# Performance work log

Hardware: AMD Instinct MI355X
Metric: run time of the kernel (lower is better)

## Reference

```python
import jax, jax.numpy as jnp
import numpy as np

B, C, H, W = 4, 64, 64, 64


def setup_inputs() -> dict:
    key = jax.random.key(0)
    k1, k2, k3, k4, k5 = jax.random.split(key, 5)
    return {
        "x": jax.random.normal(k1, (B, C, H, W), dtype=jnp.float32),
        "w_qkv": jax.random.normal(k2, (3 * C, C), dtype=jnp.float32) * (1.0 / np.sqrt(C)),
        "b_qkv": jax.random.normal(k3, (3 * C,), dtype=jnp.float32) * 0.02,
        "w_proj": jax.random.normal(k4, (C, C), dtype=jnp.float32) * (1.0 / np.sqrt(C)),
        "b_proj": jax.random.normal(k5, (C,), dtype=jnp.float32) * 0.02,
    }


def reference(x, w_qkv, b_qkv, w_proj, b_proj):
    b, c, h, w = x.shape
    xf = x.reshape(b, c, h * w)                                  # [B, C, N]
    # 1x1 Conv1d == per-position linear over channels
    qkv = jnp.einsum('oc,bcn->bon', w_qkv, xf) + b_qkv[None, :, None]  # [B, 3C, N]
    q, k, v = jnp.split(qkv, 3, axis=1)                          # each [B, C, N]
    scores = jnp.einsum('bcn,bcm->bnm', q, k) / (c ** 0.5)       # [B, N, N]
    attn = jax.nn.softmax(scores, axis=-1)
    out = jnp.einsum('bcm,bnm->bcn', v, attn)                    # [B, C, N]
    out = jnp.einsum('oc,bcn->bon', w_proj, out) + b_proj[None, :, None]
    return out.reshape(b, c, h, w) + x
```

## Files before the change

kernel.cpp:

```cpp
#include <hip/hip_runtime.h>

typedef __bf16 bf16x8 __attribute__((ext_vector_type(8)));
typedef __bf16 bf16x4 __attribute__((ext_vector_type(4)));
typedef float f32x4 __attribute__((ext_vector_type(4)));
typedef short s16x4 __attribute__((ext_vector_type(4)));

#define NB 4
#define NC 64
#define NN 4096
#define SPLIT 8

#define QSCALE (0.125f * 1.44269504088896340736f)

#if __has_builtin(__builtin_amdgcn_exp2f)
#define EXP2(x) __builtin_amdgcn_exp2f(x)
#else
#define EXP2(x) exp2f(x)
#endif

#define GLL16(src, dst)                                                  \
  __builtin_amdgcn_global_load_lds(                                      \
      (const __attribute__((address_space(1))) void*)(src),              \
      (__attribute__((address_space(3))) void*)(dst), 16, 0, 0)

__global__ __launch_bounds__(256) void qkv_kernel(
    const float* __restrict__ x, const float* __restrict__ wqkv,
    const float* __restrict__ bqkv,
    __bf16* __restrict__ Qg, __bf16* __restrict__ Kg, __bf16* __restrict__ Vg)
{
  const int tid = threadIdx.x;
  const int wave = tid >> 6;
  const int lane = tid & 63;
  const int quad = lane >> 4;
  const int l16 = lane & 15;
  const int b = blockIdx.y;
  const int tsel = blockIdx.z;
  const int n0 = blockIdx.x * 128 + wave * 32;
  const float wscale = (tsel == 0) ? QSCALE : 1.0f;

  bf16x8 wf[4][2];
#pragma unroll
  for (int ot = 0; ot < 4; ot++) {
#pragma unroll
    for (int ch = 0; ch < 2; ch++) {
      const float* wp =
          wqkv + (size_t)(tsel * 64 + ot * 16 + l16) * 64 + ch * 32 + quad * 8;
      const float4 w0 = *(const float4*)wp;
      const float4 w1 = *(const float4*)(wp + 4);
      bf16x8 f;
      f[0] = (__bf16)(w0.x * wscale); f[1] = (__bf16)(w0.y * wscale);
      f[2] = (__bf16)(w0.z * wscale); f[3] = (__bf16)(w0.w * wscale);
      f[4] = (__bf16)(w1.x * wscale); f[5] = (__bf16)(w1.y * wscale);
      f[6] = (__bf16)(w1.z * wscale); f[7] = (__bf16)(w1.w * wscale);
      wf[ot][ch] = f;
    }
  }
  float bv[4];
#pragma unroll
  for (int ot = 0; ot < 4; ot++)
    bv[ot] = bqkv[tsel * 64 + ot * 16 + l16] * wscale;

#pragma unroll
  for (int nt = 0; nt < 2; nt++) {
    const int nb = n0 + nt * 16 + l16;

    bf16x8 xf[2];
#pragma unroll
    for (int ch = 0; ch < 2; ch++) {
      float v[8];
#pragma unroll
      for (int j = 0; j < 8; j++)
        v[j] = x[(size_t)(b * 64 + ch * 32 + quad * 8 + j) * NN + nb];
      bf16x8 f;
#pragma unroll
      for (int j = 0; j < 8; j++) f[j] = (__bf16)v[j];
      xf[ch] = f;
    }

#pragma unroll
    for (int ot = 0; ot < 4; ot++) {
      f32x4 acc = (f32x4){bv[ot], bv[ot], bv[ot], bv[ot]};
      acc = __builtin_amdgcn_mfma_f32_16x16x32_bf16(xf[0], wf[ot][0], acc, 0, 0, 0);
      acc = __builtin_amdgcn_mfma_f32_16x16x32_bf16(xf[1], wf[ot][1], acc, 0, 0, 0);

      if (tsel < 2) {
        __bf16* dst = (tsel == 0) ? Qg : Kg;
#pragma unroll
        for (int r = 0; r < 4; r++)
          dst[(size_t)(b * NN + n0 + nt * 16 + quad * 4 + r) * 64 + ot * 16 + l16] =
              (__bf16)acc[r];
      } else {
        bf16x4 pv;
#pragma unroll
        for (int r = 0; r < 4; r++) pv[r] = (__bf16)acc[r];
        *(bf16x4*)(Vg + (size_t)(b * 64 + ot * 16 + l16) * NN +
                   n0 + nt * 16 + quad * 4) = pv;
      }
    }
  }
}

__global__ __launch_bounds__(256) void flash_kernel(
    const __bf16* __restrict__ Q, const __bf16* __restrict__ K,
    const __bf16* __restrict__ V, const float* __restrict__ wproj,
    __bf16* __restrict__ Opart, float* __restrict__ lpart)
{
  const int b = blockIdx.y;
  const int s = blockIdx.z;
  const int tid = threadIdx.x;
  const int wave = tid >> 6;
  const int lane = tid & 63;
  const int quad = lane >> 4;
  const int l16 = lane & 15;

  __shared__ __bf16 KB[2][64 * 64];
  __shared__ __bf16 VB[2][64 * 64];

  const int q0 = blockIdx.x * 128 + wave * 32;

  bf16x8 qf[2][2];
#pragma unroll
  for (int qt = 0; qt < 2; qt++) {
    const __bf16* qrow = Q + ((size_t)(b * NN + q0 + qt * 16 + l16)) * 64;
    qf[qt][0] = *(const bf16x8*)(qrow + quad * 8);
    qf[qt][1] = *(const bf16x8*)(qrow + 32 + quad * 8);
  }

  const int h = l16 & 7;
  const int ko0 = (quad ^ h) << 3;
  const int ko1 = ((quad + 4) ^ h) << 3;
  int vo[4];
#pragma unroll
  for (int kg = 0; kg < 4; kg++)
    vo[kg] = ((((kg << 1) + (quad >> 1)) ^ h) << 3) + ((quad & 1) << 2);

  const int c0 = wave * 128 + lane;
  const int c1 = c0 + 64;
  const int r0 = c0 >> 3, r1 = c1 >> 3;
  const int k0 = (c0 & 7) ^ (r0 & 7);
  const int k1 = (c1 & 7) ^ (r1 & 7);
  const int kbeg = s * (NN / SPLIT);
  const __bf16* Ks0 = K + ((size_t)b * NN + kbeg + r0) * 64 + k0 * 8;
  const __bf16* Ks1 = K + ((size_t)b * NN + kbeg + r1) * 64 + k1 * 8;
  const __bf16* Vs0 = V + ((size_t)(b * 64 + r0)) * NN + kbeg + k0 * 8;
  const __bf16* Vs1 = V + ((size_t)(b * 64 + r1)) * NN + kbeg + k1 * 8;
  const int db0 = wave * 128 * 8;
  const int db1 = db0 + 64 * 8;

  GLL16(Ks0, &KB[0][db0]);
  GLL16(Ks1, &KB[0][db1]);
  GLL16(Vs0, &VB[0][db0]);
  GLL16(Vs1, &VB[0][db1]);

  f32x4 acc[2][4];
#pragma unroll
  for (int qt = 0; qt < 2; qt++)
#pragma unroll
    for (int ct = 0; ct < 4; ct++) acc[qt][ct] = (f32x4){0.f, 0.f, 0.f, 0.f};
  float l[2] = {0.f, 0.f};

  __syncthreads();

  const int NT = (NN / SPLIT) / 64;
  int cur = 0;
#pragma unroll 1
  for (int t8 = 0; t8 < NT; t8++) {
    if (t8 + 1 < NT) {
      const int nb = cur ^ 1;
      const size_t kadv = (size_t)(t8 + 1) * 64 * 64;
      const int vadv = (t8 + 1) * 64;
      GLL16(Ks0 + kadv, &KB[nb][db0]);
      GLL16(Ks1 + kadv, &KB[nb][db1]);
      GLL16(Vs0 + vadv, &VB[nb][db0]);
      GLL16(Vs1 + vadv, &VB[nb][db1]);
    }
    const __bf16* Kb = KB[cur];
    const __bf16* Vb = VB[cur];

    s16x4 pk[4][2];
#pragma unroll
    for (int t = 0; t < 4; t++) {
      const __bf16* krow = Kb + (t * 16 + l16) * 64;
      const bf16x8 kf0 = *(const bf16x8*)(krow + ko0);
      const bf16x8 kf1 = *(const bf16x8*)(krow + ko1);
#pragma unroll
      for (int qt = 0; qt < 2; qt++) {
        f32x4 z = (f32x4){0.f, 0.f, 0.f, 0.f};
        z = __builtin_amdgcn_mfma_f32_16x16x32_bf16(kf0, qf[qt][0], z, 0, 0, 0);
        z = __builtin_amdgcn_mfma_f32_16x16x32_bf16(kf1, qf[qt][1], z, 0, 0, 0);
        const float p0 = EXP2(z[0]), p1 = EXP2(z[1]);
        const float p2 = EXP2(z[2]), p3 = EXP2(z[3]);
        l[qt] += (p0 + p1) + (p2 + p3);
        bf16x4 pv;
        pv[0] = (__bf16)p0; pv[1] = (__bf16)p1;
        pv[2] = (__bf16)p2; pv[3] = (__bf16)p3;
        pk[t][qt] = __builtin_bit_cast(s16x4, pv);
      }
    }

#pragma unroll
    for (int kg = 0; kg < 4; kg++) {
#pragma unroll
      for (int ct = 0; ct < 4; ct++) {
        const bf16x4 va =
            *(const bf16x4*)(Vb + (ct * 16 + l16) * 64 + vo[kg]);
        const s16x4 a = __builtin_bit_cast(s16x4, va);
        acc[0][ct] = __builtin_amdgcn_mfma_f32_16x16x16bf16_1k(
            a, pk[kg][0], acc[0][ct], 0, 0, 0);
        acc[1][ct] = __builtin_amdgcn_mfma_f32_16x16x16bf16_1k(
            a, pk[kg][1], acc[1][ct], 0, 0, 0);
      }
    }

    if (t8 + 1 < NT) __syncthreads();
    cur ^= 1;
  }

#pragma unroll
  for (int qt = 0; qt < 2; qt++) {
    float lr = l[qt];
    lr += __shfl_xor(lr, 16);
    lr += __shfl_xor(lr, 32);
    if (quad == 0)
      lpart[((size_t)(s * NB + b)) * NN + q0 + qt * 16 + l16] = lr;
  }

  s16x4 ob[2][4];
#pragma unroll
  for (int qt = 0; qt < 2; qt++)
#pragma unroll
    for (int ch = 0; ch < 4; ch++) {
      bf16x4 t;
#pragma unroll
      for (int r = 0; r < 4; r++) t[r] = (__bf16)acc[qt][ch][r];
      ob[qt][ch] = __builtin_bit_cast(s16x4, t);
    }

#pragma unroll
  for (int cot = 0; cot < 4; cot++) {
    f32x4 po[2];
    po[0] = (f32x4){0.f, 0.f, 0.f, 0.f};
    po[1] = (f32x4){0.f, 0.f, 0.f, 0.f};
#pragma unroll
    for (int ch = 0; ch < 4; ch++) {
      const float4 wv =
          *(const float4*)&wproj[(cot * 16 + l16) * 64 + ch * 16 + quad * 4];
      bf16x4 wb;
      wb[0] = (__bf16)wv.x; wb[1] = (__bf16)wv.y;
      wb[2] = (__bf16)wv.z; wb[3] = (__bf16)wv.w;
      const s16x4 a = __builtin_bit_cast(s16x4, wb);
      po[0] = __builtin_amdgcn_mfma_f32_16x16x16bf16_1k(a, ob[0][ch], po[0], 0, 0, 0);
      po[1] = __builtin_amdgcn_mfma_f32_16x16x16bf16_1k(a, ob[1][ch], po[1], 0, 0, 0);
    }
#pragma unroll
    for (int qt = 0; qt < 2; qt++)
#pragma unroll
      for (int r = 0; r < 4; r++)
        Opart[(((size_t)(s * NB + b)) * 64 + cot * 16 + quad * 4 + r) * NN +
              q0 + qt * 16 + l16] = (__bf16)po[qt][r];
  }
}

__global__ __launch_bounds__(256) void combine_kernel(
    const __bf16* __restrict__ Opart, const float* __restrict__ lpart,
    const float* __restrict__ bproj, const float* __restrict__ x,
    float* __restrict__ out)
{
  const int b = blockIdx.y;
  const int n0 = blockIdx.x * 32;
  const int tid = threadIdx.x;

  __shared__ float linv[32];
  if (tid < 32) {
    float lt = 0.f;
#pragma unroll
    for (int s = 0; s < SPLIT; s++)
      lt += lpart[((size_t)(s * NB + b)) * NN + n0 + tid];
    linv[tid] = 1.0f / lt;
  }
  __syncthreads();

  const int c = tid >> 2;
  const int n8 = (tid & 3) * 8;

  float o[8];
#pragma unroll
  for (int j = 0; j < 8; j++) o[j] = 0.f;
#pragma unroll
  for (int s = 0; s < SPLIT; s++) {
    const bf16x8 v = *(const bf16x8*)(
        Opart + (((size_t)(s * NB + b)) * 64 + c) * NN + n0 + n8);
#pragma unroll
    for (int j = 0; j < 8; j++) o[j] += (float)v[j];
  }

  const float bb = bproj[c];
  const float4 li0 = *(const float4*)&linv[n8];
  const float4 li1 = *(const float4*)&linv[n8 + 4];
  const size_t base = ((size_t)(b * 64 + c)) * NN + n0 + n8;
  const float4 x0 = *(const float4*)&x[base];
  const float4 x1 = *(const float4*)&x[base + 4];
  float4 r0, r1;
  r0.x = o[0] * li0.x + bb + x0.x;  r0.y = o[1] * li0.y + bb + x0.y;
  r0.z = o[2] * li0.z + bb + x0.z;  r0.w = o[3] * li0.w + bb + x0.w;
  r1.x = o[4] * li1.x + bb + x1.x;  r1.y = o[5] * li1.y + bb + x1.y;
  r1.z = o[6] * li1.z + bb + x1.z;  r1.w = o[7] * li1.w + bb + x1.w;
  *(float4*)&out[base] = r0;
  *(float4*)&out[base + 4] = r1;
}

extern "C" void kernel_launch(void* const* d_in, const int* in_sizes, int n_in,
                              void* d_out, int out_size, void* d_ws, size_t ws_size,
                              hipStream_t stream) {
  const float* x     = (const float*)d_in[0];
  const float* wqkv  = (const float*)d_in[1];
  const float* bqkv  = (const float*)d_in[2];
  const float* wproj = (const float*)d_in[3];
  const float* bproj = (const float*)d_in[4];
  float* out = (float*)d_out;

  char* ws = (char*)d_ws;
  __bf16* Q     = (__bf16*)(ws);
  __bf16* K     = (__bf16*)(ws + (2u << 20));
  __bf16* V     = (__bf16*)(ws + (4u << 20));
  __bf16* Opart = (__bf16*)(ws + (6u << 20));
  float*  lpart = (float*)(ws + (23u << 20));

  qkv_kernel<<<dim3(32, NB, 3), 256, 0, stream>>>(x, wqkv, bqkv, Q, K, V);
  flash_kernel<<<dim3(32, NB, SPLIT), 256, 0, stream>>>(Q, K, V, wproj,
                                                        Opart, lpart);
  combine_kernel<<<dim3(128, NB), 256, 0, stream>>>(Opart, lpart, bproj, x,
                                                    out);
}
```

Baseline: 113.7 us.

## Halve flash tile sizes: 16 queries per wave, 32-key tiles, double block count

Reduces each wave's query tile from 32 to 16 rows and the key/value tile from 64 to 32 columns, with a new LDS swizzle for the narrower V tile. The grid doubles in x (64 blocks per batch/split) to cover the same queries. The aim is more blocks and less register/LDS pressure per block for better occupancy on the GPU. The cost is less K/V reuse per load, so global-to-LDS traffic roughly doubles, and there are twice as many loop iterations and barriers.

After: 119.9 us. +5.5%, slower.

```diff
diff --git a/kernel.cpp b/kernel.cpp
--- a/kernel.cpp
+++ b/kernel.cpp
@@ -113,102 +113,88 @@
   const int quad = lane >> 4;
   const int l16 = lane & 15;
 
-  __shared__ __bf16 KB[2][64 * 64];
-  __shared__ __bf16 VB[2][64 * 64];
-
-  const int q0 = blockIdx.x * 128 + wave * 32;
-
-  bf16x8 qf[2][2];
-#pragma unroll
-  for (int qt = 0; qt < 2; qt++) {
-    const __bf16* qrow = Q + ((size_t)(b * NN + q0 + qt * 16 + l16)) * 64;
-    qf[qt][0] = *(const bf16x8*)(qrow + quad * 8);
-    qf[qt][1] = *(const bf16x8*)(qrow + 32 + quad * 8);
+  __shared__ __bf16 KB[2][32 * 64];
+  __shared__ __bf16 VB[2][64 * 32];
+
+  const int q0 = blockIdx.x * 64 + wave * 16;
+
+  bf16x8 qf[2];
+  {
+    const __bf16* qrow = Q + ((size_t)(b * NN + q0 + l16)) * 64;
+    qf[0] = *(const bf16x8*)(qrow + quad * 8);
+    qf[1] = *(const bf16x8*)(qrow + 32 + quad * 8);
   }
 
   const int h = l16 & 7;
   const int ko0 = (quad ^ h) << 3;
   const int ko1 = ((quad + 4) ^ h) << 3;
-  int vo[4];
-#pragma unroll
-  for (int kg = 0; kg < 4; kg++)
-    vo[kg] = ((((kg << 1) + (quad >> 1)) ^ h) << 3) + ((quad & 1) << 2);
-
-  const int c0 = wave * 128 + lane;
-  const int c1 = c0 + 64;
-  const int r0 = c0 >> 3, r1 = c1 >> 3;
-  const int k0 = (c0 & 7) ^ (r0 & 7);
-  const int k1 = (c1 & 7) ^ (r1 & 7);
+  const int hv = (l16 >> 1) & 3;
+  int vo[2];
+#pragma unroll
+  for (int kg = 0; kg < 2; kg++)
+    vo[kg] = ((((kg << 1) + (quad >> 1)) ^ hv) << 3) + ((quad & 1) << 2);
+
+  const int c = wave * 64 + lane;
+  const int rK = c >> 3, sK = (c & 7) ^ (rK & 7);
+  const int rV = c >> 2, sV = (c & 3) ^ ((rV >> 1) & 3);
   const int kbeg = s * (NN / SPLIT);
-  const __bf16* Ks0 = K + ((size_t)b * NN + kbeg + r0) * 64 + k0 * 8;
-  const __bf16* Ks1 = K + ((size_t)b * NN + kbeg + r1) * 64 + k1 * 8;
-  const __bf16* Vs0 = V + ((size_t)(b * 64 + r0)) * NN + kbeg + k0 * 8;
-  const __bf16* Vs1 = V + ((size_t)(b * 64 + r1)) * NN + kbeg + k1 * 8;
-  const int db0 = wave * 128 * 8;
-  const int db1 = db0 + 64 * 8;
-
-  GLL16(Ks0, &KB[0][db0]);
-  GLL16(Ks1, &KB[0][db1]);
-  GLL16(Vs0, &VB[0][db0]);
-  GLL16(Vs1, &VB[0][db1]);
-
-  f32x4 acc[2][4];
-#pragma unroll
-  for (int qt = 0; qt < 2; qt++)
-#pragma unroll
-    for (int ct = 0; ct < 4; ct++) acc[qt][ct] = (f32x4){0.f, 0.f, 0.f, 0.f};
-  float l[2] = {0.f, 0.f};
+  const __bf16* Ksrc = K + ((size_t)b * NN + kbeg + rK) * 64 + sK * 8;
+  const __bf16* Vsrc = V + ((size_t)(b * 64 + rV)) * NN + kbeg + sV * 8;
+  const int db = wave * 512;
+
+  GLL16(Ksrc, &KB[0][db]);
+  GLL16(Vsrc, &VB[0][db]);
+  Ksrc += 32 * 64;
+  Vsrc += 32;
+
+  f32x4 acc[4];
+#pragma unroll
+  for (int ct = 0; ct < 4; ct++) acc[ct] = (f32x4){0.f, 0.f, 0.f, 0.f};
+  float l = 0.f;
 
   __syncthreads();
 
-  const int NT = (NN / SPLIT) / 64;
+  const int NT = (NN / SPLIT) / 32;
   int cur = 0;
 #pragma unroll 1
   for (int t8 = 0; t8 < NT; t8++) {
     if (t8 + 1 < NT) {
       const int nb = cur ^ 1;
-      const size_t kadv = (size_t)(t8 + 1) * 64 * 64;
-      const int vadv = (t8 + 1) * 64;
-      GLL16(Ks0 + kadv, &KB[nb][db0]);
-      GLL16(Ks1 + kadv, &KB[nb][db1]);
-      GLL16(Vs0 + vadv, &VB[nb][db0]);
-      GLL16(Vs1 + vadv, &VB[nb][db1]);
+      GLL16(Ksrc, &KB[nb][db]);
+      GLL16(Vsrc, &VB[nb][db]);
+      Ksrc += 32 * 64;
+      Vsrc += 32;
     }
     const __bf16* Kb = KB[cur];
     const __bf16* Vb = VB[cur];
 
-    s16x4 pk[4][2];
-#pragma unroll
-    for (int t = 0; t < 4; t++) {
+    s16x4 pk[2];
+#pragma unroll
+    for (int t = 0; t < 2; t++) {
       const __bf16* krow = Kb + (t * 16 + l16) * 64;
       const bf16x8 kf0 = *(const bf16x8*)(krow + ko0);
       const bf16x8 kf1 = *(const bf16x8*)(krow + ko1);
-#pragma unroll
-      for (int qt = 0; qt < 2; qt++) {
-        f32x4 z = (f32x4){0.f, 0.f, 0.f, 0.f};
-        z = __builtin_amdgcn_mfma_f32_16x16x32_bf16(kf0, qf[qt][0], z, 0, 0, 0);
-        z = __builtin_amdgcn_mfma_f32_16x16x32_bf16(kf1, qf[qt][1], z, 0, 0, 0);
-        const float p0 = EXP2(z[0]), p1 = EXP2(z[1]);
-        const float p2 = EXP2(z[2]), p3 = EXP2(z[3]);
-        l[qt] += (p0 + p1) + (p2 + p3);
-        bf16x4 pv;
-        pv[0] = (__bf16)p0; pv[1] = (__bf16)p1;
-        pv[2] = (__bf16)p2; pv[3] = (__bf16)p3;
-        pk[t][qt] = __builtin_bit_cast(s16x4, pv);
-      }
-    }
-
-#pragma unroll
-    for (int kg = 0; kg < 4; kg++) {
+      f32x4 z = (f32x4){0.f, 0.f, 0.f, 0.f};
+      z = __builtin_amdgcn_mfma_f32_16x16x32_bf16(kf0, qf[0], z, 0, 0, 0);
+      z = __builtin_amdgcn_mfma_f32_16x16x32_bf16(kf1, qf[1], z, 0, 0, 0);
+      const float p0 = EXP2(z[0]), p1 = EXP2(z[1]);
+      const float p2 = EXP2(z[2]), p3 = EXP2(z[3]);
+      l += (p0 + p1) + (p2 + p3);
+      bf16x4 pv;
+      pv[0] = (__bf16)p0; pv[1] = (__bf16)p1;
+      pv[2] = (__bf16)p2; pv[3] = (__bf16)p3;
+      pk[t] = __builtin_bit_cast(s16x4, pv);
+    }
+
+#pragma unroll
+    for (int kg = 0; kg < 2; kg++) {
 #pragma unroll
       for (int ct = 0; ct < 4; ct++) {
         const bf16x4 va =
-            *(const bf16x4*)(Vb + (ct * 16 + l16) * 64 + vo[kg]);
+            *(const bf16x4*)(Vb + (ct * 16 + l16) * 32 + vo[kg]);
         const s16x4 a = __builtin_bit_cast(s16x4, va);
-        acc[0][ct] = __builtin_amdgcn_mfma_f32_16x16x16bf16_1k(
-            a, pk[kg][0], acc[0][ct], 0, 0, 0);
-        acc[1][ct] = __builtin_amdgcn_mfma_f32_16x16x16bf16_1k(
-            a, pk[kg][1], acc[1][ct], 0, 0, 0);
+        acc[ct] = __builtin_amdgcn_mfma_f32_16x16x16bf16_1k(
+            a, pk[kg], acc[ct], 0, 0, 0);
       }
     }
 
@@ -216,31 +202,26 @@
     cur ^= 1;
   }
 
-#pragma unroll
-  for (int qt = 0; qt < 2; qt++) {
-    float lr = l[qt];
+  {
+    float lr = l;
     lr += __shfl_xor(lr, 16);
     lr += __shfl_xor(lr, 32);
     if (quad == 0)
-      lpart[((size_t)(s * NB + b)) * NN + q0 + qt * 16 + l16] = lr;
-  }
-
-  s16x4 ob[2][4];
-#pragma unroll
-  for (int qt = 0; qt < 2; qt++)
-#pragma unroll
-    for (int ch = 0; ch < 4; ch++) {
-      bf16x4 t;
-#pragma unroll
-      for (int r = 0; r < 4; r++) t[r] = (__bf16)acc[qt][ch][r];
-      ob[qt][ch] = __builtin_bit_cast(s16x4, t);
-    }
+      lpart[((size_t)(s * NB + b)) * NN + q0 + l16] = lr;
+  }
+
+  s16x4 ob[4];
+#pragma unroll
+  for (int ch = 0; ch < 4; ch++) {
+    bf16x4 t;
+#pragma unroll
+    for (int r = 0; r < 4; r++) t[r] = (__bf16)acc[ch][r];
+    ob[ch] = __builtin_bit_cast(s16x4, t);
+  }
 
 #pragma unroll
   for (int cot = 0; cot < 4; cot++) {
-    f32x4 po[2];
-    po[0] = (f32x4){0.f, 0.f, 0.f, 0.f};
-    po[1] = (f32x4){0.f, 0.f, 0.f, 0.f};
+    f32x4 po = (f32x4){0.f, 0.f, 0.f, 0.f};
 #pragma unroll
     for (int ch = 0; ch < 4; ch++) {
       const float4 wv =
@@ -249,15 +230,12 @@
       wb[0] = (__bf16)wv.x; wb[1] = (__bf16)wv.y;
       wb[2] = (__bf16)wv.z; wb[3] = (__bf16)wv.w;
       const s16x4 a = __builtin_bit_cast(s16x4, wb);
-      po[0] = __builtin_amdgcn_mfma_f32_16x16x16bf16_1k(a, ob[0][ch], po[0], 0, 0, 0);
-      po[1] = __builtin_amdgcn_mfma_f32_16x16x16bf16_1k(a, ob[1][ch], po[1], 0, 0, 0);
-    }
-#pragma unroll
-    for (int qt = 0; qt < 2; qt++)
-#pragma unroll
-      for (int r = 0; r < 4; r++)
-        Opart[(((size_t)(s * NB + b)) * 64 + cot * 16 + quad * 4 + r) * NN +
-              q0 + qt * 16 + l16] = (__bf16)po[qt][r];
+      po = __builtin_amdgcn_mfma_f32_16x16x16bf16_1k(a, ob[ch], po, 0, 0, 0);
+    }
+#pragma unroll
+    for (int r = 0; r < 4; r++)
+      Opart[(((size_t)(s * NB + b)) * 64 + cot * 16 + quad * 4 + r) * NN +
+            q0 + l16] = (__bf16)po[r];
   }
 }
 
@@ -327,7 +305,7 @@
   float*  lpart = (float*)(ws + (23u << 20));
 
   qkv_kernel<<<dim3(32, NB, 3), 256, 0, stream>>>(x, wqkv, bqkv, Q, K, V);
-  flash_kernel<<<dim3(32, NB, SPLIT), 256, 0, stream>>>(Q, K, V, wproj,
+  flash_kernel<<<dim3(64, NB, SPLIT), 256, 0, stream>>>(Q, K, V, wproj,
                                                         Opart, lpart);
   combine_kernel<<<dim3(128, NB), 256, 0, stream>>>(Opart, lpart, bproj, x,
                                                     out);
```
